# Optimization experiments

Measured on AMD Instinct MI355X. Metric: run time of the kernel, lower is better.

## Reference

```python
import jax, jax.numpy as jnp
import numpy as np

B, S, D, F, E = 4, 1024, 768, 3072, 8
TOP_K = 2


def setup_inputs() -> dict:
    key = jax.random.key(0)
    k0, k1, k2, k3 = jax.random.split(key, 4)
    x = jax.random.normal(k0, (B, S, D), dtype=jnp.float32)
    w_router = jax.random.normal(k1, (D, E), dtype=jnp.float32) * 0.02
    w1 = jax.random.normal(k2, (E, D, F), dtype=jnp.float32) * 0.02
    b1 = jnp.zeros((E, F), dtype=jnp.float32)
    w2 = jax.random.normal(k3, (E, F, D), dtype=jnp.float32) * 0.02
    b2 = jnp.zeros((E, D), dtype=jnp.float32)
    return {"x": x, "w_router": w_router, "w1": w1, "b1": b1, "w2": w2, "b2": b2}


def reference(x, w_router, w1, b1, w2, b2):
    # Router: logits [B,S,E] -> softmax -> top-k -> renormalize
    router_logits = jnp.einsum('bsd,de->bse', x, w_router)
    router_probs = jax.nn.softmax(router_logits, axis=-1)
    top_k_probs, top_k_idx = jax.lax.top_k(router_probs, TOP_K)  # [B,S,K]
    top_k_probs = top_k_probs / (jnp.sum(top_k_probs, axis=-1, keepdims=True) + 1e-8)
    # Combine weights [B,S,E]: weight for expert e if selected, else 0.
    # (top-k indices are distinct, so summing one-hots over k is exact.)
    combine = jnp.sum(
        jax.nn.one_hot(top_k_idx, E, dtype=x.dtype) * top_k_probs[..., None], axis=-2)
    # Dense per-expert FFN over ALL tokens (faithful to the original masked-dense math).
    h = jax.nn.gelu(jnp.einsum('bsd,edf->ebsf', x, w1) + b1[:, None, None, :],
                    approximate=False)  # [E,B,S,F]
    expert_out = jnp.einsum('ebsf,efd->ebsd', h, w2) + b2[:, None, None, :]  # [E,B,S,D]
    output = jnp.einsum('ebsd,bse->bsd', expert_out, combine)
    return output
```

## Files before the change

### kernel.cpp

```cpp
#include <hip/hip_runtime.h>
#include <math.h>

typedef __bf16 bf16x8 __attribute__((ext_vector_type(8)));
typedef float f32x4 __attribute__((ext_vector_type(4)));

#define B_ 4
#define S_ 1024
#define D_ 768
#define F_ 3072
#define E_ 8
#define NTOK 4096
#define NSLOTP 9216

__device__ __forceinline__ void gload_lds16(const void* g, void* s) {
  __builtin_amdgcn_global_load_lds((const __attribute__((address_space(1))) void*)g,
                                   (__attribute__((address_space(3))) void*)s, 16, 0, 0);
}

__device__ __forceinline__ float gelu_f(float v) {
  float u = v * (0.7978845608f + 0.0356774081f * v * v);
  float t = 1.f - 2.f / (1.f + __expf(2.f * u));
  return 0.5f * v * (1.f + t);
}

__global__ __launch_bounds__(256) void k_router(const float* __restrict__ x,
    const float* __restrict__ wr, int* __restrict__ tki, float* __restrict__ tkw) {
  int wid = threadIdx.x >> 6, lane = threadIdx.x & 63;
  int t = blockIdx.x * 4 + wid;
  const float* xp = x + (size_t)t * D_;
  float pa[E_];
#pragma unroll
  for (int e = 0; e < E_; ++e) pa[e] = 0.f;
#pragma unroll
  for (int it = 0; it < D_ / 64; ++it) {
    int d = it * 64 + lane;
    float xv = xp[d];
    const float4* wp = (const float4*)(wr + (size_t)d * E_);
    float4 a = wp[0], b = wp[1];
    pa[0] += xv * a.x; pa[1] += xv * a.y; pa[2] += xv * a.z; pa[3] += xv * a.w;
    pa[4] += xv * b.x; pa[5] += xv * b.y; pa[6] += xv * b.z; pa[7] += xv * b.w;
  }
#pragma unroll
  for (int e = 0; e < E_; ++e) {
    float v = pa[e];
    for (int off = 32; off; off >>= 1) v += __shfl_xor(v, off);
    pa[e] = v;
  }
  if (lane == 0) {
    float m = pa[0];
#pragma unroll
    for (int e = 1; e < E_; ++e) m = fmaxf(m, pa[e]);
    float p[E_], s = 0.f;
#pragma unroll
    for (int e = 0; e < E_; ++e) { p[e] = expf(pa[e] - m); s += p[e]; }
#pragma unroll
    for (int e = 0; e < E_; ++e) p[e] = p[e] / s;
    int i0 = 0; float b0 = p[0];
#pragma unroll
    for (int e = 1; e < E_; ++e) if (p[e] > b0) { b0 = p[e]; i0 = e; }
    int i1 = -1; float b1v = -1.f;
#pragma unroll
    for (int e = 0; e < E_; ++e) if (e != i0 && p[e] > b1v) { b1v = p[e]; i1 = e; }
    float den = b0 + b1v + 1e-8f;
    tki[t * 2] = i0; tki[t * 2 + 1] = i1;
    tkw[t * 2] = b0 / den; tkw[t * 2 + 1] = b1v / den;
  }
}

__global__ __launch_bounds__(256) void k_route_all(const int* __restrict__ tki,
    int* __restrict__ stok, int* __restrict__ tslot, int* __restrict__ aoff) {
  __shared__ int cl[256][E_];
  __shared__ int tot[E_];
  __shared__ int aoffA[E_ + 1];
  int tid = threadIdx.x;
  for (int i = tid; i < NSLOTP; i += 256) stok[i] = -1;
#pragma unroll
  for (int e = 0; e < E_; ++e) cl[tid][e] = 0;
  int t0 = tid * (NTOK / 256);
#pragma unroll
  for (int i = 0; i < NTOK / 256; ++i) {
    cl[tid][tki[(t0 + i) * 2]]++;
    cl[tid][tki[(t0 + i) * 2 + 1]]++;
  }
  __syncthreads();
  if (tid < E_) {
    int run = 0;
    for (int i = 0; i < 256; ++i) { int v = cl[i][tid]; cl[i][tid] = run; run += v; }
    tot[tid] = run;
  }
  __syncthreads();
  if (tid == 0) {
    int a = 0; aoffA[0] = 0; aoff[0] = 0;
    for (int e = 0; e < E_; ++e) { a += ((tot[e] + 127) >> 7) << 7; aoffA[e + 1] = a; aoff[e + 1] = a; }
  }
  __syncthreads();
#pragma unroll
  for (int i = 0; i < NTOK / 256; ++i) {
    int t = t0 + i;
#pragma unroll
    for (int k = 0; k < 2; ++k) {
      int e = tki[t * 2 + k];
      int pos = aoffA[e] + cl[tid][e];
      cl[tid][e]++;
      stok[pos] = t;
      tslot[t * 2 + k] = pos;
    }
  }
}

__global__ __launch_bounds__(256) void k_gather(const float* __restrict__ x,
    const int* __restrict__ stok, __bf16* __restrict__ Xg) {
  int i8 = blockIdx.x * 256 + threadIdx.x;
  int flat = i8 * 8;
  int row = flat / D_;
  int col = flat - row * D_;
  int tok = stok[row];
  bf16x8 v;
  if (tok >= 0) {
    const float4* s = (const float4*)(x + (size_t)tok * D_ + col);
    float4 a = s[0], b = s[1];
    v[0] = (__bf16)a.x; v[1] = (__bf16)a.y; v[2] = (__bf16)a.z; v[3] = (__bf16)a.w;
    v[4] = (__bf16)b.x; v[5] = (__bf16)b.y; v[6] = (__bf16)b.z; v[7] = (__bf16)b.w;
  } else {
#pragma unroll
    for (int k = 0; k < 8; ++k) v[k] = (__bf16)0.f;
  }
  *(bf16x8*)(Xg + (size_t)flat) = v;
}

__global__ __launch_bounds__(256) void k_transpose(const float* __restrict__ in,
    __bf16* __restrict__ outp, int R, int C) {
  __shared__ float Ts[64][65];
  int e = blockIdx.z;
  int r0 = blockIdx.y * 64, c0 = blockIdx.x * 64;
  const float* ip = in + (size_t)e * R * C;
  int lr = threadIdx.x >> 4;
  int lc = (threadIdx.x & 15) * 4;
#pragma unroll
  for (int it = 0; it < 4; ++it) {
    int r = lr + it * 16;
    float4 v = *(const float4*)(ip + (size_t)(r0 + r) * C + c0 + lc);
    Ts[r][lc] = v.x; Ts[r][lc + 1] = v.y; Ts[r][lc + 2] = v.z; Ts[r][lc + 3] = v.w;
  }
  __syncthreads();
  int rr = (threadIdx.x & 7) * 8;
  int cc = threadIdx.x >> 3;
  __bf16* op = outp + (size_t)e * R * C + r0 + rr;
#pragma unroll
  for (int it = 0; it < 2; ++it) {
    int c = cc + it * 32;
    bf16x8 v;
#pragma unroll
    for (int i = 0; i < 8; ++i) v[i] = (__bf16)Ts[rr + i][c];
    *(bf16x8*)(op + (size_t)(c0 + c) * R) = v;
  }
}

template<int K, int N, int MODE>
__global__ __launch_bounds__(512) void k_gemm(
    const __bf16* __restrict__ A, const __bf16* __restrict__ Bt,
    const float* __restrict__ bias, const int* __restrict__ aoff,
    __bf16* __restrict__ Hout, float* __restrict__ Eout) {
  __shared__ __align__(16) __bf16 Al[128 * 32];
  __shared__ __align__(16) __bf16 Bl[256 * 32];
  constexpr int NB = N / 256;
  constexpr int NMB = NSLOTP / 128;
  constexpr int NWG = NB * NMB;
  int bswz = (blockIdx.x & 7) * (NWG / 8) + (blockIdx.x >> 3);
  int mb = bswz % NMB, nb = bswz / NMB;
  int row0 = mb * 128;
  if (row0 >= aoff[E_]) return;
  int e = 0;
#pragma unroll
  for (int q = 0; q < E_; ++q) if (row0 >= aoff[q + 1]) e = q + 1;
  const __bf16* Bp = Bt + (size_t)e * D_ * F_;
  int tid = threadIdx.x, w = tid >> 6, l = tid & 63;
  int lr = l >> 2, ls = l & 3;
  int fr = l & 15, fg = l >> 4;
  f32x4 acc[4][4] = {};
  int wrow = (w >> 2) * 64, wcol = (w & 3) * 64;
  for (int kt = 0; kt < K / 32; ++kt) {
    int k0 = kt * 32;
    {
      int rlA = w * 16 + lr;
      int sA = ls ^ ((rlA >> 1) & 3);
      gload_lds16(A + (size_t)(row0 + rlA) * K + k0 + sA * 8, Al + w * 512);
#pragma unroll
      for (int q = 0; q < 2; ++q) {
        int rlB = w * 32 + q * 16 + lr;
        int sB = ls ^ ((rlB >> 1) & 3);
        gload_lds16(Bp + (size_t)(nb * 256 + rlB) * K + k0 + sB * 8, Bl + (w * 2 + q) * 512);
      }
    }
    __syncthreads();
    bf16x8 af[4], bfr[4];
#pragma unroll
    for (int i = 0; i < 4; ++i) {
      int rl = wrow + i * 16 + fr;
      af[i] = *(const bf16x8*)(Al + rl * 32 + ((fg ^ ((rl >> 1) & 3)) << 3));
    }
#pragma unroll
    for (int j = 0; j < 4; ++j) {
      int nl = wcol + j * 16 + fr;
      bfr[j] = *(const bf16x8*)(Bl + nl * 32 + ((fg ^ ((nl >> 1) & 3)) << 3));
    }
#pragma unroll
    for (int i = 0; i < 4; ++i)
#pragma unroll
      for (int j = 0; j < 4; ++j)
        acc[i][j] = __builtin_amdgcn_mfma_f32_16x16x32_bf16(af[i], bfr[j], acc[i][j], 0, 0, 0);
    __syncthreads();
  }
  if constexpr (MODE == 0) {
#pragma unroll
    for (int j = 0; j < 4; ++j) {
      int col = nb * 256 + wcol + j * 16 + fr;
      float bv = bias[e * N + col];
#pragma unroll
      for (int i = 0; i < 4; ++i) {
#pragma unroll
        for (int r = 0; r < 4; ++r) {
          int row = row0 + wrow + i * 16 + fg * 4 + r;
          Hout[(size_t)row * N + col] = (__bf16)gelu_f(acc[i][j][r] + bv);
        }
      }
    }
  } else {
#pragma unroll
    for (int j = 0; j < 4; ++j) {
      int col = nb * 256 + wcol + j * 16 + fr;
      float bv = bias[e * N + col];
#pragma unroll
      for (int i = 0; i < 4; ++i) {
#pragma unroll
        for (int r = 0; r < 4; ++r) {
          int row = row0 + wrow + i * 16 + fg * 4 + r;
          Eout[(size_t)row * N + col] = acc[i][j][r] + bv;
        }
      }
    }
  }
}

__global__ __launch_bounds__(256) void k_combine(const float* __restrict__ Eout,
    const int* __restrict__ tslot, const float* __restrict__ tkw, float* __restrict__ out) {
  int idx = blockIdx.x * 256 + threadIdx.x;
  int t = idx / (D_ / 4);
  int c4 = (idx - t * (D_ / 4)) * 4;
  int s0 = tslot[2 * t], s1 = tslot[2 * t + 1];
  float w0 = tkw[2 * t], w1 = tkw[2 * t + 1];
  float4 a = *(const float4*)(Eout + (size_t)s0 * D_ + c4);
  float4 b = *(const float4*)(Eout + (size_t)s1 * D_ + c4);
  float4 o;
  o.x = w0 * a.x + w1 * b.x; o.y = w0 * a.y + w1 * b.y;
  o.z = w0 * a.z + w1 * b.z; o.w = w0 * a.w + w1 * b.w;
  *(float4*)(out + (size_t)t * D_ + c4) = o;
}

extern "C" void kernel_launch(void* const* d_in, const int* in_sizes, int n_in,
                              void* d_out, int out_size, void* d_ws, size_t ws_size,
                              hipStream_t stream) {
  const float* x  = (const float*)d_in[0];
  const float* wr = (const float*)d_in[1];
  const float* w1 = (const float*)d_in[2];
  const float* b1 = (const float*)d_in[3];
  const float* w2 = (const float*)d_in[4];
  const float* b2 = (const float*)d_in[5];
  float* out = (float*)d_out;

  char* ws = (char*)d_ws;
  size_t o = 0;
  __bf16* w1t = (__bf16*)(ws + o); o += (size_t)E_ * D_ * F_ * 2;
  __bf16* w2t = (__bf16*)(ws + o); o += (size_t)E_ * D_ * F_ * 2;
  __bf16* Xg  = (__bf16*)(ws + o); o += (size_t)NSLOTP * D_ * 2;
  __bf16* H   = (__bf16*)(ws + o); o += (size_t)NSLOTP * F_ * 2;
  int*   tki  = (int*)(ws + o);   o += (size_t)NTOK * 2 * 4;
  float* tkw  = (float*)(ws + o); o += (size_t)NTOK * 2 * 4;
  int*   stok = (int*)(ws + o);   o += (size_t)NSLOTP * 4;
  int*   tslot= (int*)(ws + o);   o += (size_t)NTOK * 2 * 4;
  int*   aoff = (int*)(ws + o);   o += 64;
  float* Eout = (float*)w1t;
  if (ws_size < o) return;

  k_router<<<NTOK / 4, 256, 0, stream>>>(x, wr, tki, tkw);
  k_route_all<<<1, 256, 0, stream>>>(tki, stok, tslot, aoff);
  k_gather<<<(NSLOTP * D_ / 8) / 256, 256, 0, stream>>>(x, stok, Xg);
  k_transpose<<<dim3(F_ / 64, D_ / 64, E_), 256, 0, stream>>>(w1, w1t, D_, F_);
  k_transpose<<<dim3(D_ / 64, F_ / 64, E_), 256, 0, stream>>>(w2, w2t, F_, D_);
  k_gemm<D_, F_, 0><<<(F_ / 256) * (NSLOTP / 128), 512, 0, stream>>>(
      Xg, w1t, b1, aoff, H, nullptr);
  k_gemm<F_, D_, 1><<<(D_ / 256) * (NSLOTP / 128), 512, 0, stream>>>(
      H, w2t, b2, aoff, nullptr, Eout);
  k_combine<<<NTOK * (D_ / 4) / 256, 256, 0, stream>>>(Eout, tslot, tkw, out);
}
```

Measured before the change: 232.0 us.

## Triple-buffer expert GEMM LDS stages with async prefetch and retuned tiles

Rewrites the grouped expert GEMM mainloop to use three LDS buffers. Global-to-LDS loads for tile k+2 are issued ahead of compute, and explicit vmcnt waits replace the full __syncthreads on every k-step, so memory latency overlaps with the MFMA work. The kernel is templated on N-tile and wave layout. The up-projection now uses 512-wide N tiles with a 2x4 wave grid, and the down-projection uses a 1x4 wave grid of 256 threads. Raised wave priority around the MFMAs is also added. The costs are much more LDS per block, effectively one block per CU, larger accumulator register footprints, and fewer, narrower blocks for the second GEMM, which may leave CUs underused.

```diff
diff --git a/kernel.cpp b/kernel.cpp
--- a/kernel.cpp
+++ b/kernel.cpp
@@ -15,6 +15,15 @@
 __device__ __forceinline__ void gload_lds16(const void* g, void* s) {
   __builtin_amdgcn_global_load_lds((const __attribute__((address_space(1))) void*)g,
                                    (__attribute__((address_space(3))) void*)s, 16, 0, 0);
+}
+
+template<int N> __device__ __forceinline__ void wait_vmcnt() {
+  if constexpr (N == 0)       asm volatile("s_waitcnt vmcnt(0)" ::: "memory");
+  else if constexpr (N == 5)  asm volatile("s_waitcnt vmcnt(5)" ::: "memory");
+  else if constexpr (N == 6)  asm volatile("s_waitcnt vmcnt(6)" ::: "memory");
+  else if constexpr (N == 10) asm volatile("s_waitcnt vmcnt(10)" ::: "memory");
+  else if constexpr (N == 12) asm volatile("s_waitcnt vmcnt(12)" ::: "memory");
+  else static_assert(N == 0, "unhandled vmcnt");
 }
 
 __device__ __forceinline__ float gelu_f(float v) {
@@ -156,16 +165,29 @@
   }
 }
 
-template<int K, int N, int MODE>
-__global__ __launch_bounds__(512) void k_gemm(
+template<int K, int N, int BN, int WM, int WN, int MODE>
+__global__ __launch_bounds__(WM * WN * 64, 1) void k_gemm(
     const __bf16* __restrict__ A, const __bf16* __restrict__ Bt,
     const float* __restrict__ bias, const int* __restrict__ aoff,
     __bf16* __restrict__ Hout, float* __restrict__ Eout) {
-  __shared__ __align__(16) __bf16 Al[128 * 32];
-  __shared__ __align__(16) __bf16 Bl[256 * 32];
-  constexpr int NB = N / 256;
+  constexpr int BM = 128;
+  constexpr int NW = WM * WN;
+  constexpr int NT = NW * 64;
+  constexpr int ASZ = BM * 32;
+  constexpr int BSZ = BN * 32;
+  constexpr int QA = (BM / 16) / NW;
+  constexpr int QB = (BN / 16) / NW;
+  constexpr int L = QA + QB;
+  constexpr int MI = (BM / WM) / 16;
+  constexpr int NJ = (BN / WN) / 16;
+  constexpr int NK = K / 32;
+  constexpr int NB = N / BN;
   constexpr int NMB = NSLOTP / 128;
   constexpr int NWG = NB * NMB;
+
+  __shared__ __align__(16) __bf16 Als[3 * ASZ];
+  __shared__ __align__(16) __bf16 Bls[3 * BSZ];
+
   int bswz = (blockIdx.x & 7) * (NWG / 8) + (blockIdx.x >> 3);
   int mb = bswz % NMB, nb = bswz / NMB;
   int row0 = mb * 128;
@@ -174,67 +196,90 @@
 #pragma unroll
   for (int q = 0; q < E_; ++q) if (row0 >= aoff[q + 1]) e = q + 1;
   const __bf16* Bp = Bt + (size_t)e * D_ * F_;
+
   int tid = threadIdx.x, w = tid >> 6, l = tid & 63;
   int lr = l >> 2, ls = l & 3;
   int fr = l & 15, fg = l >> 4;
-  f32x4 acc[4][4] = {};
-  int wrow = (w >> 2) * 64, wcol = (w & 3) * 64;
-  for (int kt = 0; kt < K / 32; ++kt) {
+  int wr = w / WN, wc = w % WN;
+
+  auto STAGE = [&](int kt, int b) {
     int k0 = kt * 32;
-    {
-      int rlA = w * 16 + lr;
-      int sA = ls ^ ((rlA >> 1) & 3);
-      gload_lds16(A + (size_t)(row0 + rlA) * K + k0 + sA * 8, Al + w * 512);
-#pragma unroll
-      for (int q = 0; q < 2; ++q) {
-        int rlB = w * 32 + q * 16 + lr;
-        int sB = ls ^ ((rlB >> 1) & 3);
-        gload_lds16(Bp + (size_t)(nb * 256 + rlB) * K + k0 + sB * 8, Bl + (w * 2 + q) * 512);
-      }
-    }
-    __syncthreads();
-    bf16x8 af[4], bfr[4];
-#pragma unroll
-    for (int i = 0; i < 4; ++i) {
-      int rl = wrow + i * 16 + fr;
-      af[i] = *(const bf16x8*)(Al + rl * 32 + ((fg ^ ((rl >> 1) & 3)) << 3));
-    }
-#pragma unroll
-    for (int j = 0; j < 4; ++j) {
-      int nl = wcol + j * 16 + fr;
-      bfr[j] = *(const bf16x8*)(Bl + nl * 32 + ((fg ^ ((nl >> 1) & 3)) << 3));
-    }
-#pragma unroll
-    for (int i = 0; i < 4; ++i)
-#pragma unroll
-      for (int j = 0; j < 4; ++j)
+#pragma unroll
+    for (int q = 0; q < QA; ++q) {
+      int idx = w * QA + q;
+      int row = idx * 16 + lr;
+      int slot = ls ^ ((row >> 1) & 3);
+      gload_lds16(A + (size_t)(row0 + row) * K + k0 + slot * 8,
+                  Als + b * ASZ + idx * 512);
+    }
+#pragma unroll
+    for (int q = 0; q < QB; ++q) {
+      int idx = w * QB + q;
+      int row = idx * 16 + lr;
+      int slot = ls ^ ((row >> 1) & 3);
+      gload_lds16(Bp + (size_t)(nb * BN + row) * K + k0 + slot * 8,
+                  Bls + b * BSZ + idx * 512);
+    }
+  };
+
+  f32x4 acc[MI][NJ] = {};
+  STAGE(0, 0);
+  STAGE(1, 1);
+  int cb = 0, ct = 2;
+  for (int t = 0; t < NK; ++t) {
+    if (t + 2 < NK)      { STAGE(t + 2, ct); wait_vmcnt<2 * L>(); }
+    else if (t + 1 < NK) { wait_vmcnt<L>(); }
+    else                 { wait_vmcnt<0>(); }
+    __builtin_amdgcn_sched_barrier(0);
+    __builtin_amdgcn_s_barrier();
+    __builtin_amdgcn_sched_barrier(0);
+    bf16x8 af[MI], bfr[NJ];
+#pragma unroll
+    for (int i = 0; i < MI; ++i) {
+      int rl = wr * (BM / WM) + i * 16 + fr;
+      af[i] = *(const bf16x8*)(Als + cb * ASZ + rl * 32 + ((fg ^ ((rl >> 1) & 3)) << 3));
+    }
+#pragma unroll
+    for (int j = 0; j < NJ; ++j) {
+      int nl = wc * (BN / WN) + j * 16 + fr;
+      bfr[j] = *(const bf16x8*)(Bls + cb * BSZ + nl * 32 + ((fg ^ ((nl >> 1) & 3)) << 3));
+    }
+    __builtin_amdgcn_s_setprio(1);
+#pragma unroll
+    for (int i = 0; i < MI; ++i)
+#pragma unroll
+      for (int j = 0; j < NJ; ++j)
         acc[i][j] = __builtin_amdgcn_mfma_f32_16x16x32_bf16(af[i], bfr[j], acc[i][j], 0, 0, 0);
-    __syncthreads();
-  }
+    __builtin_amdgcn_s_setprio(0);
+    __builtin_amdgcn_s_barrier();
+    cb = (cb == 2) ? 0 : cb + 1;
+    ct = (ct == 2) ? 0 : ct + 1;
+  }
+
   if constexpr (MODE == 0) {
 #pragma unroll
-    for (int j = 0; j < 4; ++j) {
-      int col = nb * 256 + wcol + j * 16 + fr;
+    for (int j = 0; j < NJ; ++j) {
+      int col = nb * BN + wc * (BN / WN) + j * 16 + fr;
       float bv = bias[e * N + col];
 #pragma unroll
-      for (int i = 0; i < 4; ++i) {
+      for (int i = 0; i < MI; ++i) {
 #pragma unroll
         for (int r = 0; r < 4; ++r) {
-          int row = row0 + wrow + i * 16 + fg * 4 + r;
+          int row = row0 + wr * (BM / WM) + i * 16 + fg * 4 + r;
           Hout[(size_t)row * N + col] = (__bf16)gelu_f(acc[i][j][r] + bv);
         }
       }
     }
   } else {
 #pragma unroll
-    for (int j = 0; j < 4; ++j) {
-      int col = nb * 256 + wcol + j * 16 + fr;
+    for (int j = 0; j < NJ; ++j) {
+      int col = nb * BN + wc * (BN / WN) + j * 16 + fr;
       float bv = bias[e * N + col];
 #pragma unroll
-      for (int i = 0; i < 4; ++i) {
+      for (int i = 0; i < MI; ++i) {
 #pragma unroll
         for (int r = 0; r < 4; ++r) {
-          int row = row0 + wrow + i * 16 + fg * 4 + r;
+          int row = row0 + wr * (BM / WM) + i * 16 + fg * 4 + r;
           Eout[(size_t)row * N + col] = acc[i][j][r] + bv;
         }
       }
@@ -287,9 +332,9 @@
   k_gather<<<(NSLOTP * D_ / 8) / 256, 256, 0, stream>>>(x, stok, Xg);
   k_transpose<<<dim3(F_ / 64, D_ / 64, E_), 256, 0, stream>>>(w1, w1t, D_, F_);
   k_transpose<<<dim3(D_ / 64, F_ / 64, E_), 256, 0, stream>>>(w2, w2t, F_, D_);
-  k_gemm<D_, F_, 0><<<(F_ / 256) * (NSLOTP / 128), 512, 0, stream>>>(
+  k_gemm<D_, F_, 512, 2, 4, 0><<<(F_ / 512) * (NSLOTP / 128), 512, 0, stream>>>(
       Xg, w1t, b1, aoff, H, nullptr);
-  k_gemm<F_, D_, 1><<<(D_ / 256) * (NSLOTP / 128), 512, 0, stream>>>(
+  k_gemm<F_, D_, 256, 1, 4, 1><<<(D_ / 256) * (NSLOTP / 128), 256, 0, stream>>>(
       H, w2t, b2, aoff, nullptr, Eout);
   k_combine<<<NTOK * (D_ / 4) / 256, 256, 0, stream>>>(Eout, tslot, tkw, out);
 }
```

New measurement: 263.7 us. +13.7%, slower.

## Double-buffer GEMM LDS tiles and split-K the second expert GEMM

Applied to the files above, without the earlier changes.

The GEMM kernel now double-buffers its A/B LDS tiles, issuing the next K-slice's global-to-LDS loads before the MFMAs on the current slice, and uses raw barriers with explicit waitcnt. The second GEMM (K=3072, only 3 column blocks) is split along K into two halves written to separate fp32 buffers, which doubles the workgroup count. The combine kernel sums those two partials. This trades extra workspace and an extra fp32 partial write and read for more parallelism and overlap of loads with compute. Split-K only runs when the workspace is large enough.

```diff
diff --git a/kernel.cpp b/kernel.cpp
--- a/kernel.cpp
+++ b/kernel.cpp
@@ -156,65 +156,90 @@
   }
 }
 
-template<int K, int N, int MODE>
-__global__ __launch_bounds__(512) void k_gemm(
+template<int KST, int N, int MODE, int KSPLIT>
+__global__ __launch_bounds__(512, 4) void k_gemm(
     const __bf16* __restrict__ A, const __bf16* __restrict__ Bt,
     const float* __restrict__ bias, const int* __restrict__ aoff,
-    __bf16* __restrict__ Hout, float* __restrict__ Eout) {
-  __shared__ __align__(16) __bf16 Al[128 * 32];
-  __shared__ __align__(16) __bf16 Bl[256 * 32];
-  constexpr int NB = N / 256;
+    __bf16* __restrict__ Hout, float* __restrict__ E0, float* __restrict__ E1) {
+  constexpr int BN = 256;
+  constexpr int ASZ = 128 * 32;
+  constexpr int BSZ = BN * 32;
+  constexpr int NK = KST / 32 / KSPLIT;
+  constexpr int NB = N / BN;
   constexpr int NMB = NSLOTP / 128;
-  constexpr int NWG = NB * NMB;
+  constexpr int NWGB = NB * NMB;
+  constexpr int NWG = NWGB * KSPLIT;
+
+  __shared__ __align__(16) __bf16 Als[2 * ASZ];
+  __shared__ __align__(16) __bf16 Bls[2 * BSZ];
+
   int bswz = (blockIdx.x & 7) * (NWG / 8) + (blockIdx.x >> 3);
-  int mb = bswz % NMB, nb = bswz / NMB;
+  int kh = bswz / NWGB;
+  int rem = bswz % NWGB;
+  int mb = rem % NMB, nb = rem / NMB;
   int row0 = mb * 128;
   if (row0 >= aoff[E_]) return;
   int e = 0;
 #pragma unroll
   for (int q = 0; q < E_; ++q) if (row0 >= aoff[q + 1]) e = q + 1;
   const __bf16* Bp = Bt + (size_t)e * D_ * F_;
+  int kbase = kh * (KST / KSPLIT);
+
   int tid = threadIdx.x, w = tid >> 6, l = tid & 63;
   int lr = l >> 2, ls = l & 3;
   int fr = l & 15, fg = l >> 4;
+  int wrow = (w >> 2) * 64, wcol = (w & 3) * 64;
+
+  auto STAGE = [&](int kt, int b) {
+    int k0 = kbase + kt * 32;
+    {
+      int rowA = w * 16 + lr;
+      int sA = ls ^ ((rowA >> 1) & 3);
+      gload_lds16(A + (size_t)(row0 + rowA) * KST + k0 + sA * 8, Als + b * ASZ + w * 512);
+    }
+#pragma unroll
+    for (int q = 0; q < 2; ++q) {
+      int idx = w * 2 + q;
+      int rowB = idx * 16 + lr;
+      int sB = ls ^ ((rowB >> 1) & 3);
+      gload_lds16(Bp + (size_t)(nb * BN + rowB) * KST + k0 + sB * 8, Bls + b * BSZ + idx * 512);
+    }
+  };
+
   f32x4 acc[4][4] = {};
-  int wrow = (w >> 2) * 64, wcol = (w & 3) * 64;
-  for (int kt = 0; kt < K / 32; ++kt) {
-    int k0 = kt * 32;
-    {
-      int rlA = w * 16 + lr;
-      int sA = ls ^ ((rlA >> 1) & 3);
-      gload_lds16(A + (size_t)(row0 + rlA) * K + k0 + sA * 8, Al + w * 512);
-#pragma unroll
-      for (int q = 0; q < 2; ++q) {
-        int rlB = w * 32 + q * 16 + lr;
-        int sB = ls ^ ((rlB >> 1) & 3);
-        gload_lds16(Bp + (size_t)(nb * 256 + rlB) * K + k0 + sB * 8, Bl + (w * 2 + q) * 512);
-      }
-    }
-    __syncthreads();
+  STAGE(0, 0);
+  asm volatile("s_waitcnt vmcnt(0)" ::: "memory");
+  __builtin_amdgcn_sched_barrier(0);
+  __builtin_amdgcn_s_barrier();
+  for (int t = 0; t < NK; ++t) {
+    int cur = t & 1;
+    if (t + 1 < NK) STAGE(t + 1, cur ^ 1);
+    __builtin_amdgcn_sched_barrier(0);
     bf16x8 af[4], bfr[4];
 #pragma unroll
     for (int i = 0; i < 4; ++i) {
       int rl = wrow + i * 16 + fr;
-      af[i] = *(const bf16x8*)(Al + rl * 32 + ((fg ^ ((rl >> 1) & 3)) << 3));
+      af[i] = *(const bf16x8*)(Als + cur * ASZ + rl * 32 + ((fg ^ ((rl >> 1) & 3)) << 3));
     }
 #pragma unroll
     for (int j = 0; j < 4; ++j) {
       int nl = wcol + j * 16 + fr;
-      bfr[j] = *(const bf16x8*)(Bl + nl * 32 + ((fg ^ ((nl >> 1) & 3)) << 3));
+      bfr[j] = *(const bf16x8*)(Bls + cur * BSZ + nl * 32 + ((fg ^ ((nl >> 1) & 3)) << 3));
     }
 #pragma unroll
     for (int i = 0; i < 4; ++i)
 #pragma unroll
       for (int j = 0; j < 4; ++j)
         acc[i][j] = __builtin_amdgcn_mfma_f32_16x16x32_bf16(af[i], bfr[j], acc[i][j], 0, 0, 0);
-    __syncthreads();
-  }
+    __builtin_amdgcn_sched_barrier(0);
+    asm volatile("s_waitcnt vmcnt(0)" ::: "memory");
+    __builtin_amdgcn_s_barrier();
+  }
+
   if constexpr (MODE == 0) {
 #pragma unroll
     for (int j = 0; j < 4; ++j) {
-      int col = nb * 256 + wcol + j * 16 + fr;
+      int col = nb * BN + wcol + j * 16 + fr;
       float bv = bias[e * N + col];
 #pragma unroll
       for (int i = 0; i < 4; ++i) {
@@ -226,34 +251,45 @@
       }
     }
   } else {
+    float* Ep = (kh == 0) ? E0 : E1;
 #pragma unroll
     for (int j = 0; j < 4; ++j) {
-      int col = nb * 256 + wcol + j * 16 + fr;
-      float bv = bias[e * N + col];
+      int col = nb * BN + wcol + j * 16 + fr;
+      float bv = (kh == 0) ? bias[e * N + col] : 0.f;
 #pragma unroll
       for (int i = 0; i < 4; ++i) {
 #pragma unroll
         for (int r = 0; r < 4; ++r) {
           int row = row0 + wrow + i * 16 + fg * 4 + r;
-          Eout[(size_t)row * N + col] = acc[i][j][r] + bv;
+          Ep[(size_t)row * N + col] = acc[i][j][r] + bv;
         }
       }
     }
   }
 }
 
-__global__ __launch_bounds__(256) void k_combine(const float* __restrict__ Eout,
-    const int* __restrict__ tslot, const float* __restrict__ tkw, float* __restrict__ out) {
+__global__ __launch_bounds__(256) void k_combine(const float* __restrict__ E0,
+    const float* __restrict__ E1, const int* __restrict__ tslot,
+    const float* __restrict__ tkw, float* __restrict__ out) {
   int idx = blockIdx.x * 256 + threadIdx.x;
   int t = idx / (D_ / 4);
   int c4 = (idx - t * (D_ / 4)) * 4;
   int s0 = tslot[2 * t], s1 = tslot[2 * t + 1];
   float w0 = tkw[2 * t], w1 = tkw[2 * t + 1];
-  float4 a = *(const float4*)(Eout + (size_t)s0 * D_ + c4);
-  float4 b = *(const float4*)(Eout + (size_t)s1 * D_ + c4);
+  float4 a = *(const float4*)(E0 + (size_t)s0 * D_ + c4);
+  float4 b = *(const float4*)(E0 + (size_t)s1 * D_ + c4);
   float4 o;
-  o.x = w0 * a.x + w1 * b.x; o.y = w0 * a.y + w1 * b.y;
-  o.z = w0 * a.z + w1 * b.z; o.w = w0 * a.w + w1 * b.w;
+  if (E1) {
+    float4 a1 = *(const float4*)(E1 + (size_t)s0 * D_ + c4);
+    float4 b1 = *(const float4*)(E1 + (size_t)s1 * D_ + c4);
+    o.x = w0 * (a.x + a1.x) + w1 * (b.x + b1.x);
+    o.y = w0 * (a.y + a1.y) + w1 * (b.y + b1.y);
+    o.z = w0 * (a.z + a1.z) + w1 * (b.z + b1.z);
+    o.w = w0 * (a.w + a1.w) + w1 * (b.w + b1.w);
+  } else {
+    o.x = w0 * a.x + w1 * b.x; o.y = w0 * a.y + w1 * b.y;
+    o.z = w0 * a.z + w1 * b.z; o.w = w0 * a.w + w1 * b.w;
+  }
   *(float4*)(out + (size_t)t * D_ + c4) = o;
 }
 
@@ -271,25 +307,34 @@
   char* ws = (char*)d_ws;
   size_t o = 0;
   __bf16* w1t = (__bf16*)(ws + o); o += (size_t)E_ * D_ * F_ * 2;
+  __bf16* Xg  = (__bf16*)(ws + o); o += (size_t)NSLOTP * D_ * 2;
   __bf16* w2t = (__bf16*)(ws + o); o += (size_t)E_ * D_ * F_ * 2;
-  __bf16* Xg  = (__bf16*)(ws + o); o += (size_t)NSLOTP * D_ * 2;
   __bf16* H   = (__bf16*)(ws + o); o += (size_t)NSLOTP * F_ * 2;
   int*   tki  = (int*)(ws + o);   o += (size_t)NTOK * 2 * 4;
   float* tkw  = (float*)(ws + o); o += (size_t)NTOK * 2 * 4;
   int*   stok = (int*)(ws + o);   o += (size_t)NSLOTP * 4;
   int*   tslot= (int*)(ws + o);   o += (size_t)NTOK * 2 * 4;
   int*   aoff = (int*)(ws + o);   o += 64;
-  float* Eout = (float*)w1t;
+  float* E0   = (float*)w1t;
+  float* E1   = (float*)(ws + o);
+  size_t oE1  = o + (size_t)NSLOTP * D_ * 4;
   if (ws_size < o) return;
+  bool split = (ws_size >= oE1);
 
   k_router<<<NTOK / 4, 256, 0, stream>>>(x, wr, tki, tkw);
   k_route_all<<<1, 256, 0, stream>>>(tki, stok, tslot, aoff);
   k_gather<<<(NSLOTP * D_ / 8) / 256, 256, 0, stream>>>(x, stok, Xg);
   k_transpose<<<dim3(F_ / 64, D_ / 64, E_), 256, 0, stream>>>(w1, w1t, D_, F_);
   k_transpose<<<dim3(D_ / 64, F_ / 64, E_), 256, 0, stream>>>(w2, w2t, F_, D_);
-  k_gemm<D_, F_, 0><<<(F_ / 256) * (NSLOTP / 128), 512, 0, stream>>>(
-      Xg, w1t, b1, aoff, H, nullptr);
-  k_gemm<F_, D_, 1><<<(D_ / 256) * (NSLOTP / 128), 512, 0, stream>>>(
-      H, w2t, b2, aoff, nullptr, Eout);
-  k_combine<<<NTOK * (D_ / 4) / 256, 256, 0, stream>>>(Eout, tslot, tkw, out);
-}
+  k_gemm<D_, F_, 0, 1><<<(F_ / 256) * (NSLOTP / 128), 512, 0, stream>>>(
+      Xg, w1t, b1, aoff, H, nullptr, nullptr);
+  if (split) {
+    k_gemm<F_, D_, 1, 2><<<2 * (D_ / 256) * (NSLOTP / 128), 512, 0, stream>>>(
+        H, w2t, b2, aoff, nullptr, E0, E1);
+    k_combine<<<NTOK * (D_ / 4) / 256, 256, 0, stream>>>(E0, E1, tslot, tkw, out);
+  } else {
+    k_gemm<F_, D_, 1, 1><<<(D_ / 256) * (NSLOTP / 128), 512, 0, stream>>>(
+        H, w2t, b2, aoff, nullptr, E0, nullptr);
+    k_combine<<<NTOK * (D_ / 4) / 256, 256, 0, stream>>>(E0, nullptr, tslot, tkw, out);
+  }
+}
```

Measured after the change: 212.9 us. 8.2% less time.
